# Performance work log

Hardware: AMD Instinct MI355X
Metric: run time of the kernel (lower is better)

The kernel has to match this reference:

```python
import jax, jax.numpy as jnp
import numpy as np

N = 100000          # num_nodes
E = 1250000         # num_edges
H = 64              # node_hidden_size
T = 2               # num_rounds


def setup_inputs() -> dict:
    key = jax.random.key(0)
    ks = jax.random.split(key, 10)
    s = 0.1  # init scale for weights
    return {
        "x": jax.random.normal(ks[0], (N, H), dtype=jnp.float32),
        "edge_index": jax.random.randint(ks[1], (2, E), 0, N, dtype=jnp.int64),
        "edge_attr": jax.random.normal(ks[2], (E, 1), dtype=jnp.float32),
        # message layers: Linear(2H+1 -> H), one per round
        "msg_W": jax.random.normal(ks[3], (T, H, 2 * H + 1), dtype=jnp.float32) * s,
        "msg_b": jax.random.normal(ks[4], (T, H), dtype=jnp.float32) * s,
        # GRUCell params, gate order (r, z, n) as in torch
        "gru_Wih": jax.random.normal(ks[5], (T, 3 * H, H), dtype=jnp.float32) * s,
        "gru_bih": jax.random.normal(ks[6], (T, 3 * H), dtype=jnp.float32) * s,
        "gru_Whh": jax.random.normal(ks[7], (T, 3 * H, H), dtype=jnp.float32) * s,
        "gru_bhh": jax.random.normal(ks[8], (T, 3 * H), dtype=jnp.float32) * s,
    }


def _gru_cell(inp, h, Wih, bih, Whh, bhh):
    # torch.nn.GRUCell math, gate order r, z, n
    gi = inp @ Wih.T + bih   # [N, 3H]
    gh = h @ Whh.T + bhh     # [N, 3H]
    i_r, i_z, i_n = jnp.split(gi, 3, axis=1)
    h_r, h_z, h_n = jnp.split(gh, 3, axis=1)
    r = jax.nn.sigmoid(i_r + h_r)
    z = jax.nn.sigmoid(i_z + h_z)
    n = jnp.tanh(i_n + r * h_n)
    return (1.0 - z) * n + z * h


def reference(x, edge_index, edge_attr, msg_W, msg_b, gru_Wih, gru_bih, gru_Whh, gru_bhh):
    row, col = edge_index[0], edge_index[1]
    num_rounds = msg_W.shape[0]
    for t in range(num_rounds):
        src = x[row]    # [E, H]
        dest = x[col]   # [E, H]
        m_input = jnp.concatenate([dest, src, edge_attr], axis=1)  # [E, 2H+1]
        messages = m_input @ msg_W[t].T + msg_b[t]                 # [E, H]
        agg = jax.ops.segment_sum(messages, row, num_segments=x.shape[0])  # [N, H]
        x = _gru_cell(agg, x, gru_Wih[t], gru_bih[t], gru_Whh[t], gru_bhh[t])
    return x
```

## Files before the change

### kernel.cpp

```cpp
#include <hip/hip_runtime.h>
#include <hip/hip_bf16.h>
#include <hip/hip_fp16.h>

#define H 64
#define CAP 48

typedef __attribute__((ext_vector_type(8))) short short8;
typedef __attribute__((ext_vector_type(4))) float float4v;

__device__ __forceinline__ short f2bf_bits(float f) {
    union { __hip_bfloat16 b; short s; } u;
    u.b = __float2bfloat16(f);
    return u.s;
}
__device__ __forceinline__ float bf2f(unsigned short s) {
    union { unsigned int u; float f; } v;
    v.u = ((unsigned int)s) << 16;
    return v.f;
}
__device__ __forceinline__ void split8(const float* __restrict__ p,
                                       short8& hi, short8& lo) {
    float4v f0 = *(const float4v*)p;
    float4v f1 = *(const float4v*)(p + 4);
#pragma unroll
    for (int j = 0; j < 8; j++) {
        float f = (j < 4) ? f0[j] : f1[j - 4];
        short h = f2bf_bits(f);
        float fh = bf2f((unsigned short)h);
        hi[j] = h;
        lo[j] = f2bf_bits(f - fh);
    }
}
__device__ __forceinline__ void zero8(short8& hi, short8& lo) {
#pragma unroll
    for (int j = 0; j < 8; j++) { hi[j] = 0; lo[j] = 0; }
}

#define MFMA(a, b, c) __builtin_amdgcn_mfma_f32_16x16x32_bf16(a, b, c, 0, 0, 0)

__global__ __launch_bounds__(64) void prep_msg(
    const float* __restrict__ msg_W, short* __restrict__ frag)
{
    const int slot = blockIdx.x & 15, t = blockIdx.x >> 4, lane = threadIdx.x;
    const int tile = slot >> 1, ks = slot & 1;
    const float* W = msg_W + (size_t)t * H * 129;
    const int wrow = (tile & 3) * 16 + (lane & 15);
    const int coff = (tile < 4) ? 0 : 64;
    const int kq = (lane >> 4) * 8;
    short8 hi, lo;
    split8(W + (size_t)wrow * 129 + coff + ks * 32 + kq, hi, lo);
    short8* out = (short8*)(frag + (size_t)t * 16384);
    out[slot * 64 + lane] = hi;
    out[16 * 64 + slot * 64 + lane] = lo;
}

__global__ __launch_bounds__(64) void prep_gru(
    const float* __restrict__ Wih, const float* __restrict__ Whh,
    short* __restrict__ frag)
{
    const int slot = blockIdx.x % 48, t = blockIdx.x / 48, lane = threadIdx.x;
    const int tile = slot >> 1, ks = slot & 1;
    const int kq = (lane >> 4) * 8;
    const float* Wp = (tile < 12)
        ? (Wih + (size_t)t * 192 * H + ((size_t)(tile * 16 + (lane & 15))) * H)
        : (Whh + (size_t)t * 192 * H + ((size_t)((tile - 12) * 16 + (lane & 15))) * H);
    short8 hi, lo;
    split8(Wp + ks * 32 + kq, hi, lo);
    short8* out = (short8*)(frag + (size_t)t * 49152);
    out[slot * 64 + lane] = hi;
    out[48 * 64 + slot * 64 + lane] = lo;
}

__global__ __launch_bounds__(256) void count_cast(
    const int* __restrict__ row, int* __restrict__ deg, int* __restrict__ lpos,
    int E, int EB,
    const float* __restrict__ x_in, __half* __restrict__ xh, int NH8)
{
    if ((int)blockIdx.x < EB) {
        int e = blockIdx.x * 256 + threadIdx.x;
        if (e < E) lpos[e] = atomicAdd(&deg[row[e]], 1);
    } else {
        int i = (blockIdx.x - EB) * 256 + threadIdx.x;
        if (i < NH8) {
            const float* p = x_in + (size_t)i * 8;
            float4v f0 = *(const float4v*)p;
            float4v f1 = *(const float4v*)(p + 4);
            short8 hv;
#pragma unroll
            for (int u = 0; u < 8; u++) {
                float f = (u < 4) ? f0[u] : f1[u - 4];
                hv[u] = __half_as_short(__float2half(f));
            }
            *(short8*)(xh + (size_t)i * 8) = hv;
        }
    }
}

__global__ __launch_bounds__(256) void scatter_bucket(
    const int* __restrict__ row, const int* __restrict__ col,
    const float* __restrict__ attr, const int* __restrict__ lpos,
    int2* __restrict__ edata, int E)
{
    int e = blockIdx.x * 256 + threadIdx.x;
    if (e < E) {
        int p = lpos[e];
        if (p < CAP) {
            int2 v;
            v.x = col[e];
            v.y = __float_as_int(attr[e]);
            edata[(size_t)row[e] * CAP + p] = v;
        }
    }
}

__global__ __launch_bounds__(256) void aggregate(
    const int* __restrict__ deg, const int2* __restrict__ edata,
    const __half* __restrict__ xh,
    short* __restrict__ s_hi, short* __restrict__ s_lo,
    float2* __restrict__ asum2, int N)
{
    const int tid = threadIdx.x, lane = tid & 63, wv = tid >> 6;
    const int n = blockIdx.x * 4 + wv;
    if (n >= N) return;
    int cnt = deg[n];
    if (cnt > CAP) cnt = CAP;
    int2 ed = make_int2(0, 0);
    if (lane < cnt) ed = edata[(size_t)n * CAP + lane];
    const int g = lane >> 3;
    const int cl = lane & 7;
    float acc[8] = {0.f, 0.f, 0.f, 0.f, 0.f, 0.f, 0.f, 0.f};
    float aacc = 0.f;
    for (int j = 0; j < cnt; j += 8) {
        const int idx = j + g;
        int   c = __shfl(ed.x, idx, 64);
        float a = __shfl(__int_as_float(ed.y), idx, 64);
        short8 hv = *(const short8*)(xh + (size_t)c * H + cl * 8);
        if (idx < cnt) {
            aacc += a;
#pragma unroll
            for (int u = 0; u < 8; u++)
                acc[u] += __half2float(__ushort_as_half((unsigned short)hv[u]));
        }
    }
#pragma unroll
    for (int off = 8; off < 64; off <<= 1) {
        aacc += __shfl_xor(aacc, off, 64);
#pragma unroll
        for (int u = 0; u < 8; u++) acc[u] += __shfl_xor(acc[u], off, 64);
    }
    if (lane < 8) {
        short8 hi8, lo8;
#pragma unroll
        for (int u = 0; u < 8; u++) {
            float v = acc[u];
            short h = f2bf_bits(v);
            hi8[u] = h;
            lo8[u] = f2bf_bits(v - bf2f((unsigned short)h));
        }
        *(short8*)(s_hi + (size_t)n * H + lane * 8) = hi8;
        *(short8*)(s_lo + (size_t)n * H + lane * 8) = lo8;
    }
    if (lane == 0) asum2[n] = make_float2(aacc, (float)cnt);
}

#define FSLOT(mt, ks, arr, hl) (((((mt) * 2 + (ks)) * 2 + (arr)) * 2 + (hl)))
__global__ __launch_bounds__(256) void fused_msg_gru(
    const short* __restrict__ s_hi, const short* __restrict__ s_lo,
    const float2* __restrict__ asum2,
    const float* __restrict__ xf,
    float* __restrict__ x, __half* __restrict__ xh,
    const short* __restrict__ mfrag, const short* __restrict__ gfrag,
    const float* __restrict__ Wt, const float* __restrict__ mb,
    const float* __restrict__ bih, const float* __restrict__ bhh,
    int N, int write_xh)
{
    __shared__ short8 afrag[32 * 64];
    const int tid = threadIdx.x, lane = tid & 63, q = tid >> 6;
    const int base = blockIdx.x * 64;
    const int arow = lane & 15;
    const int kq = (lane >> 4) * 8;
    const short8* mhi = (const short8*)mfrag;
    const short8* mlo = mhi + 16 * 64;
    const short8* ghi = (const short8*)gfrag;
    const short8* glo = ghi + 48 * 64;

    {
        const int m = base + q * 16 + arow;
#pragma unroll
        for (int ks = 0; ks < 2; ks++) {
            short8 hi, lo;
            if (m < N) {
                hi = *(const short8*)(s_hi + (size_t)m * H + ks * 32 + kq);
                lo = *(const short8*)(s_lo + (size_t)m * H + ks * 32 + kq);
            } else zero8(hi, lo);
            afrag[FSLOT(q, ks, 0, 0) * 64 + lane] = hi;
            afrag[FSLOT(q, ks, 0, 1) * 64 + lane] = lo;
            if (m < N) split8(xf + (size_t)m * H + ks * 32 + kq, hi, lo);
            else       zero8(hi, lo);
            afrag[FSLOT(q, ks, 1, 0) * 64 + lane] = hi;
            afrag[FSLOT(q, ks, 1, 1) * 64 + lane] = lo;
        }
    }
    __syncthreads();

    float4v accd[4], accs[4];
#pragma unroll
    for (int mt = 0; mt < 4; mt++) {
        accd[mt] = (float4v){0.f, 0.f, 0.f, 0.f};
        accs[mt] = (float4v){0.f, 0.f, 0.f, 0.f};
    }
#pragma unroll
    for (int ks = 0; ks < 2; ks++) {
        short8 ah[4], al[4];
#pragma unroll
        for (int mt = 0; mt < 4; mt++) {
            ah[mt] = afrag[FSLOT(mt, ks, 0, 0) * 64 + lane];
            al[mt] = afrag[FSLOT(mt, ks, 0, 1) * 64 + lane];
        }
        const int sd = q * 2 + ks;
        short8 bh = mhi[sd * 64 + lane];
        short8 bl = mlo[sd * 64 + lane];
#pragma unroll
        for (int mt = 0; mt < 4; mt++) {
            accd[mt] = MFMA(ah[mt], bh, accd[mt]);
            accd[mt] = MFMA(al[mt], bh, accd[mt]);
            accd[mt] = MFMA(ah[mt], bl, accd[mt]);
        }
#pragma unroll
        for (int mt = 0; mt < 4; mt++) {
            ah[mt] = afrag[FSLOT(mt, ks, 1, 0) * 64 + lane];
            al[mt] = afrag[FSLOT(mt, ks, 1, 1) * 64 + lane];
        }
        const int ss = (4 + q) * 2 + ks;
        short8 ch = mhi[ss * 64 + lane];
        short8 cl = mlo[ss * 64 + lane];
#pragma unroll
        for (int mt = 0; mt < 4; mt++) {
            accs[mt] = MFMA(ah[mt], ch, accs[mt]);
            accs[mt] = MFMA(al[mt], ch, accs[mt]);
            accs[mt] = MFMA(ah[mt], cl, accs[mt]);
        }
    }

    const int colb = lane & 15;
    const int rq4 = (lane >> 4) * 4;
    const int j = q * 16 + colb;
    const int ksW  = q >> 1;
    const int quad = (j >> 3) & 3;
    const int elem = j & 7;
    float vv[4][4];
    {
        const float bj = mb[j];
        const float wa = Wt[(size_t)j * 129 + 128];
#pragma unroll
        for (int mt = 0; mt < 4; mt++) {
#pragma unroll
            for (int r = 0; r < 4; r++) {
                const int m = base + mt * 16 + rq4 + r;
                float v = 0.f;
                if (m < N) {
                    float2 da = asum2[m];
                    v = accd[mt][r] + da.y * (accs[mt][r] + bj) + wa * da.x;
                }
                vv[mt][r] = v;
            }
        }
    }
    __syncthreads();

    {
        short* af = (short*)afrag;
#pragma unroll
        for (int mt = 0; mt < 4; mt++) {
#pragma unroll
            for (int r = 0; r < 4; r++) {
                float v = vv[mt][r];
                short hi = f2bf_bits(v);
                float fh = bf2f((unsigned short)hi);
                short lo = f2bf_bits(v - fh);
                const int lane2 = (rq4 + r) | (quad << 4);
                af[(FSLOT(mt, ksW, 0, 0) * 64 + lane2) * 8 + elem] = hi;
                af[(FSLOT(mt, ksW, 0, 1) * 64 + lane2) * 8 + elem] = lo;
            }
        }
    }
    __syncthreads();

    float4v acc[6][4];
#pragma unroll
    for (int g = 0; g < 6; g++)
#pragma unroll
        for (int mt = 0; mt < 4; mt++) acc[g][mt] = (float4v){0.f, 0.f, 0.f, 0.f};

#pragma unroll
    for (int ks = 0; ks < 2; ks++) {
        short8 ah[4], al[4];
#pragma unroll
        for (int mt = 0; mt < 4; mt++) {
            ah[mt] = afrag[FSLOT(mt, ks, 0, 0) * 64 + lane];
            al[mt] = afrag[FSLOT(mt, ks, 0, 1) * 64 + lane];
        }
#pragma unroll
        for (int g = 0; g < 3; g++) {
            const int si = (g * 4 + q) * 2 + ks;
            short8 bh = ghi[si * 64 + lane];
            short8 bl = glo[si * 64 + lane];
#pragma unroll
            for (int mt = 0; mt < 4; mt++) {
                acc[g][mt] = MFMA(ah[mt], bh, acc[g][mt]);
                acc[g][mt] = MFMA(al[mt], bh, acc[g][mt]);
                acc[g][mt] = MFMA(ah[mt], bl, acc[g][mt]);
            }
        }
#pragma unroll
        for (int mt = 0; mt < 4; mt++) {
            ah[mt] = afrag[FSLOT(mt, ks, 1, 0) * 64 + lane];
            al[mt] = afrag[FSLOT(mt, ks, 1, 1) * 64 + lane];
        }
#pragma unroll
        for (int g = 0; g < 3; g++) {
            const int sh = (12 + g * 4 + q) * 2 + ks;
            short8 bh = ghi[sh * 64 + lane];
            short8 bl = glo[sh * 64 + lane];
#pragma unroll
            for (int mt = 0; mt < 4; mt++) {
                acc[3 + g][mt] = MFMA(ah[mt], bh, acc[3 + g][mt]);
                acc[3 + g][mt] = MFMA(al[mt], bh, acc[3 + g][mt]);
                acc[3 + g][mt] = MFMA(ah[mt], bl, acc[3 + g][mt]);
            }
        }
    }

    const float b_ir = bih[j], b_iz = bih[64 + j], b_in = bih[128 + j];
    const float b_hr = bhh[j], b_hz = bhh[64 + j], b_hn = bhh[128 + j];
    const short* af = (const short*)afrag;
#pragma unroll
    for (int mt = 0; mt < 4; mt++) {
#pragma unroll
        for (int r = 0; r < 4; r++) {
            const int m = base + mt * 16 + rq4 + r;
            if (m >= N) continue;
            float ir = acc[0][mt][r] + b_ir;
            float iz = acc[1][mt][r] + b_iz;
            float in_ = acc[2][mt][r] + b_in;
            float hr = acc[3][mt][r] + b_hr;
            float hz = acc[4][mt][r] + b_hz;
            float hn = acc[5][mt][r] + b_hn;
            float rr = 1.f / (1.f + __expf(-(ir + hr)));
            float zz = 1.f / (1.f + __expf(-(iz + hz)));
            float e2 = __expf(2.f * (in_ + rr * hn));
            float nn = 1.f - 2.f / (e2 + 1.f);
            const int lane2 = (rq4 + r) | (quad << 4);
            float hold = bf2f((unsigned short)af[(FSLOT(mt, ksW, 1, 0) * 64 + lane2) * 8 + elem])
                       + bf2f((unsigned short)af[(FSLOT(mt, ksW, 1, 1) * 64 + lane2) * 8 + elem]);
            float out = (1.f - zz) * nn + zz * hold;
            x[(size_t)m * H + j] = out;
            if (write_xh) xh[(size_t)m * H + j] = __float2half(out);
        }
    }
}

extern "C" void kernel_launch(void* const* d_in, const int* in_sizes, int n_in,
                              void* d_out, int out_size, void* d_ws, size_t ws_size,
                              hipStream_t stream) {
    const float* x_in  = (const float*)d_in[0];
    const int*   ei    = (const int*)d_in[1];
    const float* attr  = (const float*)d_in[2];
    const float* msg_W = (const float*)d_in[3];
    const float* msg_b = (const float*)d_in[4];
    const float* Wih   = (const float*)d_in[5];
    const float* bih   = (const float*)d_in[6];
    const float* Whh   = (const float*)d_in[7];
    const float* bhh   = (const float*)d_in[8];

    const int N = in_sizes[0] / H;
    const int E = in_sizes[2];
    const int T = in_sizes[4] / H;
    const int* row = ei;
    const int* col = ei + E;

    float*  x       = (float*)d_out;
    short*  s_hi    = (short*)d_ws;
    short*  s_lo    = s_hi + (size_t)N * H;
    int*    lpos    = (int*)s_lo;
    __half* xh      = (__half*)(s_lo + (size_t)N * H);
    float2* asum2   = (float2*)(xh + (size_t)N * H);
    int*    deg     = (int*)(asum2 + N);
    int2*   edata   = (int2*)(deg + N);
    short*  msgfrag = (short*)(edata + (size_t)N * CAP);
    short*  grufrag = msgfrag + (size_t)T * 16384;

    const int eb  = (E + 255) / 256;
    const int nh8 = (N * H) / 8;
    const int cb  = (nh8 + 255) / 256;

    hipMemsetAsync(deg, 0, (size_t)N * sizeof(int), stream);

    prep_msg<<<T * 16, 64, 0, stream>>>(msg_W, msgfrag);
    prep_gru<<<T * 48, 64, 0, stream>>>(Wih, Whh, grufrag);

    count_cast<<<eb + cb, 256, 0, stream>>>(row, deg, lpos, E, eb, x_in, xh, nh8);
    scatter_bucket<<<eb, 256, 0, stream>>>(row, col, attr, lpos, edata, E);

    const int nbq        = (N + 63) / 64;
    const int agg_blocks = (N + 3) / 4;

    for (int t = 0; t < T; t++) {
        aggregate<<<agg_blocks, 256, 0, stream>>>(
            deg, edata, xh, s_hi, s_lo, asum2, N);
        fused_msg_gru<<<nbq, 256, 0, stream>>>(
            s_hi, s_lo, asum2,
            (t == 0) ? x_in : x, x, xh,
            msgfrag + (size_t)t * 16384, grufrag + (size_t)t * 49152,
            msg_W + (size_t)t * H * (2 * H + 1), msg_b + (size_t)t * H,
            bih + (size_t)t * 3 * H, bhh + (size_t)t * 3 * H,
            N, (t + 1 < T) ? 1 : 0);
    }
}
```

Before: 361.5 us.

## Merge prep kernels, use 8-lane-per-node aggregation, make msg-GRU kernel per-wave

The weight-fragment prep kernels are folded into the degree-count launch, and the fp16 cast of x moves into the scatter launch, cutting the launch count. Aggregation now gives each node 8 lanes that loop over its edges sequentially, replacing a 64-lane wave per node with shuffles and a cross-lane reduction. The fused message+GRU kernel is restructured so each wave owns 16 rows and all output columns, keeping A fragments in registers, using per-wave LDS scratch instead of block-wide shared fragments and __syncthreads, and reading the old hidden state directly from fp32 x. The trade-offs are more weight-fragment global loads per wave, longer serial per-lane loops for high-degree nodes, and dropped __restrict__ on the x pointers.

```diff
diff --git a/kernel.cpp b/kernel.cpp
--- a/kernel.cpp
+++ b/kernel.cpp
@@ -18,8 +18,7 @@
     v.u = ((unsigned int)s) << 16;
     return v.f;
 }
-__device__ __forceinline__ void split8(const float* __restrict__ p,
-                                       short8& hi, short8& lo) {
+__device__ __forceinline__ void split8(const float* p, short8& hi, short8& lo) {
     float4v f0 = *(const float4v*)p;
     float4v f1 = *(const float4v*)(p + 4);
 #pragma unroll
@@ -38,47 +37,65 @@
 
 #define MFMA(a, b, c) __builtin_amdgcn_mfma_f32_16x16x32_bf16(a, b, c, 0, 0, 0)
 
-__global__ __launch_bounds__(64) void prep_msg(
-    const float* __restrict__ msg_W, short* __restrict__ frag)
-{
-    const int slot = blockIdx.x & 15, t = blockIdx.x >> 4, lane = threadIdx.x;
-    const int tile = slot >> 1, ks = slot & 1;
-    const float* W = msg_W + (size_t)t * H * 129;
-    const int wrow = (tile & 3) * 16 + (lane & 15);
-    const int coff = (tile < 4) ? 0 : 64;
-    const int kq = (lane >> 4) * 8;
-    short8 hi, lo;
-    split8(W + (size_t)wrow * 129 + coff + ks * 32 + kq, hi, lo);
-    short8* out = (short8*)(frag + (size_t)t * 16384);
-    out[slot * 64 + lane] = hi;
-    out[16 * 64 + slot * 64 + lane] = lo;
-}
-
-__global__ __launch_bounds__(64) void prep_gru(
-    const float* __restrict__ Wih, const float* __restrict__ Whh,
-    short* __restrict__ frag)
-{
-    const int slot = blockIdx.x % 48, t = blockIdx.x / 48, lane = threadIdx.x;
-    const int tile = slot >> 1, ks = slot & 1;
-    const int kq = (lane >> 4) * 8;
-    const float* Wp = (tile < 12)
-        ? (Wih + (size_t)t * 192 * H + ((size_t)(tile * 16 + (lane & 15))) * H)
-        : (Whh + (size_t)t * 192 * H + ((size_t)((tile - 12) * 16 + (lane & 15))) * H);
-    short8 hi, lo;
-    split8(Wp + ks * 32 + kq, hi, lo);
-    short8* out = (short8*)(frag + (size_t)t * 49152);
-    out[slot * 64 + lane] = hi;
-    out[48 * 64 + slot * 64 + lane] = lo;
-}
-
-__global__ __launch_bounds__(256) void count_cast(
+__global__ __launch_bounds__(256) void count_prep(
     const int* __restrict__ row, int* __restrict__ deg, int* __restrict__ lpos,
     int E, int EB,
+    const float* __restrict__ msg_W,
+    const float* __restrict__ Wih, const float* __restrict__ Whh,
+    short* __restrict__ msgfrag, short* __restrict__ grufrag, int T)
+{
+    if ((int)blockIdx.x < EB) {
+        int e = blockIdx.x * 256 + threadIdx.x;
+        if (e < E) lpos[e] = atomicAdd(&deg[row[e]], 1);
+        return;
+    }
+    const int lane = threadIdx.x & 63;
+    int unit = (blockIdx.x - EB) * 4 + (threadIdx.x >> 6);
+    const int kq = (lane >> 4) * 8;
+    if (unit < T * 16) {
+        const int slot = unit & 15, t = unit >> 4;
+        const int tile = slot >> 1, ks = slot & 1;
+        const float* W = msg_W + (size_t)t * H * 129;
+        const int wrow = (tile & 3) * 16 + (lane & 15);
+        const int coff = (tile < 4) ? 0 : 64;
+        short8 hi, lo;
+        split8(W + (size_t)wrow * 129 + coff + ks * 32 + kq, hi, lo);
+        short8* out = (short8*)(msgfrag + (size_t)t * 16384);
+        out[slot * 64 + lane] = hi;
+        out[16 * 64 + slot * 64 + lane] = lo;
+    } else {
+        unit -= T * 16;
+        if (unit >= T * 48) return;
+        const int slot = unit % 48, t = unit / 48;
+        const int tile = slot >> 1, ks = slot & 1;
+        const float* Wp = (tile < 12)
+            ? (Wih + (size_t)t * 192 * H + ((size_t)(tile * 16 + (lane & 15))) * H)
+            : (Whh + (size_t)t * 192 * H + ((size_t)((tile - 12) * 16 + (lane & 15))) * H);
+        short8 hi, lo;
+        split8(Wp + ks * 32 + kq, hi, lo);
+        short8* out = (short8*)(grufrag + (size_t)t * 49152);
+        out[slot * 64 + lane] = hi;
+        out[48 * 64 + slot * 64 + lane] = lo;
+    }
+}
+
+__global__ __launch_bounds__(256) void scatter_cast(
+    const int* __restrict__ row, const int* __restrict__ col,
+    const float* __restrict__ attr, const int* __restrict__ lpos,
+    int2* __restrict__ edata, int E, int EB,
     const float* __restrict__ x_in, __half* __restrict__ xh, int NH8)
 {
     if ((int)blockIdx.x < EB) {
         int e = blockIdx.x * 256 + threadIdx.x;
-        if (e < E) lpos[e] = atomicAdd(&deg[row[e]], 1);
+        if (e < E) {
+            int p = lpos[e];
+            if (p < CAP) {
+                int2 v;
+                v.x = col[e];
+                v.y = __float_as_int(attr[e]);
+                edata[(size_t)row[e] * CAP + p] = v;
+            }
+        }
     } else {
         int i = (blockIdx.x - EB) * 256 + threadIdx.x;
         if (i < NH8) {
@@ -96,23 +113,6 @@
     }
 }
 
-__global__ __launch_bounds__(256) void scatter_bucket(
-    const int* __restrict__ row, const int* __restrict__ col,
-    const float* __restrict__ attr, const int* __restrict__ lpos,
-    int2* __restrict__ edata, int E)
-{
-    int e = blockIdx.x * 256 + threadIdx.x;
-    if (e < E) {
-        int p = lpos[e];
-        if (p < CAP) {
-            int2 v;
-            v.x = col[e];
-            v.y = __float_as_int(attr[e]);
-            edata[(size_t)row[e] * CAP + p] = v;
-        }
-    }
-}
-
 __global__ __launch_bounds__(256) void aggregate(
     const int* __restrict__ deg, const int2* __restrict__ edata,
     const __half* __restrict__ xh,
@@ -120,35 +120,22 @@
     float2* __restrict__ asum2, int N)
 {
     const int tid = threadIdx.x, lane = tid & 63, wv = tid >> 6;
-    const int n = blockIdx.x * 4 + wv;
-    if (n >= N) return;
-    int cnt = deg[n];
-    if (cnt > CAP) cnt = CAP;
-    int2 ed = make_int2(0, 0);
-    if (lane < cnt) ed = edata[(size_t)n * CAP + lane];
-    const int g = lane >> 3;
-    const int cl = lane & 7;
+    const int g = lane >> 3, cl = lane & 7;
+    const int n = (blockIdx.x * 4 + wv) * 8 + g;
+    int cnt = 0;
+    if (n < N) { cnt = deg[n]; if (cnt > CAP) cnt = CAP; }
+    const int2* ebase = edata + (size_t)n * CAP;
     float acc[8] = {0.f, 0.f, 0.f, 0.f, 0.f, 0.f, 0.f, 0.f};
     float aacc = 0.f;
-    for (int j = 0; j < cnt; j += 8) {
-        const int idx = j + g;
-        int   c = __shfl(ed.x, idx, 64);
-        float a = __shfl(__int_as_float(ed.y), idx, 64);
-        short8 hv = *(const short8*)(xh + (size_t)c * H + cl * 8);
-        if (idx < cnt) {
-            aacc += a;
-#pragma unroll
-            for (int u = 0; u < 8; u++)
-                acc[u] += __half2float(__ushort_as_half((unsigned short)hv[u]));
-        }
-    }
-#pragma unroll
-    for (int off = 8; off < 64; off <<= 1) {
-        aacc += __shfl_xor(aacc, off, 64);
-#pragma unroll
-        for (int u = 0; u < 8; u++) acc[u] += __shfl_xor(acc[u], off, 64);
-    }
-    if (lane < 8) {
+    for (int j = 0; j < cnt; j++) {
+        int2 ed = ebase[j];
+        aacc += __int_as_float(ed.y);
+        short8 hv = *(const short8*)(xh + (size_t)ed.x * H + cl * 8);
+#pragma unroll
+        for (int u = 0; u < 8; u++)
+            acc[u] += __half2float(__ushort_as_half((unsigned short)hv[u]));
+    }
+    if (n < N) {
         short8 hi8, lo8;
 #pragma unroll
         for (int u = 0; u < 8; u++) {
@@ -157,202 +144,136 @@
             hi8[u] = h;
             lo8[u] = f2bf_bits(v - bf2f((unsigned short)h));
         }
-        *(short8*)(s_hi + (size_t)n * H + lane * 8) = hi8;
-        *(short8*)(s_lo + (size_t)n * H + lane * 8) = lo8;
-    }
-    if (lane == 0) asum2[n] = make_float2(aacc, (float)cnt);
-}
-
-#define FSLOT(mt, ks, arr, hl) (((((mt) * 2 + (ks)) * 2 + (arr)) * 2 + (hl)))
+        *(short8*)(s_hi + (size_t)n * H + cl * 8) = hi8;
+        *(short8*)(s_lo + (size_t)n * H + cl * 8) = lo8;
+        if (cl == 0) asum2[n] = make_float2(aacc, (float)cnt);
+    }
+}
+
 __global__ __launch_bounds__(256) void fused_msg_gru(
     const short* __restrict__ s_hi, const short* __restrict__ s_lo,
     const float2* __restrict__ asum2,
-    const float* __restrict__ xf,
-    float* __restrict__ x, __half* __restrict__ xh,
+    const float* xf,
+    float* x, __half* __restrict__ xh,
     const short* __restrict__ mfrag, const short* __restrict__ gfrag,
     const float* __restrict__ Wt, const float* __restrict__ mb,
     const float* __restrict__ bih, const float* __restrict__ bhh,
     int N, int write_xh)
 {
-    __shared__ short8 afrag[32 * 64];
-    const int tid = threadIdx.x, lane = tid & 63, q = tid >> 6;
-    const int base = blockIdx.x * 64;
+    __shared__ float scratch[4][16 * 68];
+    const int tid = threadIdx.x, lane = tid & 63, wv = tid >> 6;
+    const int base = blockIdx.x * 64 + wv * 16;
+    if (base >= N) return;
     const int arow = lane & 15;
     const int kq = (lane >> 4) * 8;
+    const int colb = lane & 15;
+    const int rq4 = (lane >> 4) * 4;
+    const int m_a = base + arow;
+    const bool mv = (m_a < N);
     const short8* mhi = (const short8*)mfrag;
     const short8* mlo = mhi + 16 * 64;
     const short8* ghi = (const short8*)gfrag;
     const short8* glo = ghi + 48 * 64;
 
-    {
-        const int m = base + q * 16 + arow;
-#pragma unroll
-        for (int ks = 0; ks < 2; ks++) {
-            short8 hi, lo;
-            if (m < N) {
-                hi = *(const short8*)(s_hi + (size_t)m * H + ks * 32 + kq);
-                lo = *(const short8*)(s_lo + (size_t)m * H + ks * 32 + kq);
-            } else zero8(hi, lo);
-            afrag[FSLOT(q, ks, 0, 0) * 64 + lane] = hi;
-            afrag[FSLOT(q, ks, 0, 1) * 64 + lane] = lo;
-            if (m < N) split8(xf + (size_t)m * H + ks * 32 + kq, hi, lo);
-            else       zero8(hi, lo);
-            afrag[FSLOT(q, ks, 1, 0) * 64 + lane] = hi;
-            afrag[FSLOT(q, ks, 1, 1) * 64 + lane] = lo;
-        }
-    }
-    __syncthreads();
+    short8 sfh[2], sfl[2], xfh[2], xfl[2];
+#pragma unroll
+    for (int ks = 0; ks < 2; ks++) {
+        if (mv) {
+            sfh[ks] = *(const short8*)(s_hi + (size_t)m_a * H + ks * 32 + kq);
+            sfl[ks] = *(const short8*)(s_lo + (size_t)m_a * H + ks * 32 + kq);
+            split8(xf + (size_t)m_a * H + ks * 32 + kq, xfh[ks], xfl[ks]);
+        } else { zero8(sfh[ks], sfl[ks]); zero8(xfh[ks], xfl[ks]); }
+    }
+    float2 da[4];
+#pragma unroll
+    for (int r = 0; r < 4; r++) {
+        const int m = base + rq4 + r;
+        da[r] = (m < N) ? asum2[m] : make_float2(0.f, 0.f);
+    }
 
     float4v accd[4], accs[4];
 #pragma unroll
-    for (int mt = 0; mt < 4; mt++) {
-        accd[mt] = (float4v){0.f, 0.f, 0.f, 0.f};
-        accs[mt] = (float4v){0.f, 0.f, 0.f, 0.f};
+    for (int ct = 0; ct < 4; ct++) {
+        accd[ct] = (float4v){0.f, 0.f, 0.f, 0.f};
+        accs[ct] = (float4v){0.f, 0.f, 0.f, 0.f};
     }
 #pragma unroll
     for (int ks = 0; ks < 2; ks++) {
-        short8 ah[4], al[4];
-#pragma unroll
-        for (int mt = 0; mt < 4; mt++) {
-            ah[mt] = afrag[FSLOT(mt, ks, 0, 0) * 64 + lane];
-            al[mt] = afrag[FSLOT(mt, ks, 0, 1) * 64 + lane];
-        }
-        const int sd = q * 2 + ks;
-        short8 bh = mhi[sd * 64 + lane];
-        short8 bl = mlo[sd * 64 + lane];
-#pragma unroll
-        for (int mt = 0; mt < 4; mt++) {
-            accd[mt] = MFMA(ah[mt], bh, accd[mt]);
-            accd[mt] = MFMA(al[mt], bh, accd[mt]);
-            accd[mt] = MFMA(ah[mt], bl, accd[mt]);
-        }
-#pragma unroll
-        for (int mt = 0; mt < 4; mt++) {
-            ah[mt] = afrag[FSLOT(mt, ks, 1, 0) * 64 + lane];
-            al[mt] = afrag[FSLOT(mt, ks, 1, 1) * 64 + lane];
-        }
-        const int ss = (4 + q) * 2 + ks;
-        short8 ch = mhi[ss * 64 + lane];
-        short8 cl = mlo[ss * 64 + lane];
-#pragma unroll
-        for (int mt = 0; mt < 4; mt++) {
-            accs[mt] = MFMA(ah[mt], ch, accs[mt]);
-            accs[mt] = MFMA(al[mt], ch, accs[mt]);
-            accs[mt] = MFMA(ah[mt], cl, accs[mt]);
-        }
-    }
-
-    const int colb = lane & 15;
-    const int rq4 = (lane >> 4) * 4;
-    const int j = q * 16 + colb;
-    const int ksW  = q >> 1;
-    const int quad = (j >> 3) & 3;
-    const int elem = j & 7;
-    float vv[4][4];
-    {
+#pragma unroll
+        for (int ct = 0; ct < 4; ct++) {
+            short8 bh = mhi[(ct * 2 + ks) * 64 + lane];
+            short8 bl = mlo[(ct * 2 + ks) * 64 + lane];
+            accd[ct] = MFMA(sfh[ks], bh, accd[ct]);
+            accd[ct] = MFMA(sfl[ks], bh, accd[ct]);
+            accd[ct] = MFMA(sfh[ks], bl, accd[ct]);
+            short8 ch = mhi[((4 + ct) * 2 + ks) * 64 + lane];
+            short8 cl8 = mlo[((4 + ct) * 2 + ks) * 64 + lane];
+            accs[ct] = MFMA(xfh[ks], ch, accs[ct]);
+            accs[ct] = MFMA(xfl[ks], ch, accs[ct]);
+            accs[ct] = MFMA(xfh[ks], cl8, accs[ct]);
+        }
+    }
+
+    float* scr = scratch[wv];
+#pragma unroll
+    for (int ct = 0; ct < 4; ct++) {
+        const int j = ct * 16 + colb;
         const float bj = mb[j];
         const float wa = Wt[(size_t)j * 129 + 128];
 #pragma unroll
-        for (int mt = 0; mt < 4; mt++) {
-#pragma unroll
-            for (int r = 0; r < 4; r++) {
-                const int m = base + mt * 16 + rq4 + r;
-                float v = 0.f;
-                if (m < N) {
-                    float2 da = asum2[m];
-                    v = accd[mt][r] + da.y * (accs[mt][r] + bj) + wa * da.x;
-                }
-                vv[mt][r] = v;
+        for (int r = 0; r < 4; r++) {
+            float v = accd[ct][r] + da[r].y * (accs[ct][r] + bj) + da[r].x * wa;
+            scr[(rq4 + r) * 68 + j] = v;
+        }
+    }
+    asm volatile("s_waitcnt lgkmcnt(0)" ::: "memory");
+    short8 agh[2], agl[2];
+#pragma unroll
+    for (int ks = 0; ks < 2; ks++)
+        split8(scr + arow * 68 + ks * 32 + kq, agh[ks], agl[ks]);
+
+#pragma unroll
+    for (int ct = 0; ct < 4; ct++) {
+        float4v ai[3], ao[3];
+#pragma unroll
+        for (int g2 = 0; g2 < 3; g2++) {
+            ai[g2] = (float4v){0.f, 0.f, 0.f, 0.f};
+            ao[g2] = (float4v){0.f, 0.f, 0.f, 0.f};
+        }
+#pragma unroll
+        for (int ks = 0; ks < 2; ks++) {
+#pragma unroll
+            for (int g2 = 0; g2 < 3; g2++) {
+                short8 bh = ghi[((g2 * 4 + ct) * 2 + ks) * 64 + lane];
+                short8 bl = glo[((g2 * 4 + ct) * 2 + ks) * 64 + lane];
+                ai[g2] = MFMA(agh[ks], bh, ai[g2]);
+                ai[g2] = MFMA(agl[ks], bh, ai[g2]);
+                ai[g2] = MFMA(agh[ks], bl, ai[g2]);
+                short8 hh = ghi[((12 + g2 * 4 + ct) * 2 + ks) * 64 + lane];
+                short8 hl = glo[((12 + g2 * 4 + ct) * 2 + ks) * 64 + lane];
+                ao[g2] = MFMA(xfh[ks], hh, ao[g2]);
+                ao[g2] = MFMA(xfl[ks], hh, ao[g2]);
+                ao[g2] = MFMA(xfh[ks], hl, ao[g2]);
             }
         }
-    }
-    __syncthreads();
-
-    {
-        short* af = (short*)afrag;
-#pragma unroll
-        for (int mt = 0; mt < 4; mt++) {
-#pragma unroll
-            for (int r = 0; r < 4; r++) {
-                float v = vv[mt][r];
-                short hi = f2bf_bits(v);
-                float fh = bf2f((unsigned short)hi);
-                short lo = f2bf_bits(v - fh);
-                const int lane2 = (rq4 + r) | (quad << 4);
-                af[(FSLOT(mt, ksW, 0, 0) * 64 + lane2) * 8 + elem] = hi;
-                af[(FSLOT(mt, ksW, 0, 1) * 64 + lane2) * 8 + elem] = lo;
-            }
-        }
-    }
-    __syncthreads();
-
-    float4v acc[6][4];
-#pragma unroll
-    for (int g = 0; g < 6; g++)
-#pragma unroll
-        for (int mt = 0; mt < 4; mt++) acc[g][mt] = (float4v){0.f, 0.f, 0.f, 0.f};
-
-#pragma unroll
-    for (int ks = 0; ks < 2; ks++) {
-        short8 ah[4], al[4];
-#pragma unroll
-        for (int mt = 0; mt < 4; mt++) {
-            ah[mt] = afrag[FSLOT(mt, ks, 0, 0) * 64 + lane];
-            al[mt] = afrag[FSLOT(mt, ks, 0, 1) * 64 + lane];
-        }
-#pragma unroll
-        for (int g = 0; g < 3; g++) {
-            const int si = (g * 4 + q) * 2 + ks;
-            short8 bh = ghi[si * 64 + lane];
-            short8 bl = glo[si * 64 + lane];
-#pragma unroll
-            for (int mt = 0; mt < 4; mt++) {
-                acc[g][mt] = MFMA(ah[mt], bh, acc[g][mt]);
-                acc[g][mt] = MFMA(al[mt], bh, acc[g][mt]);
-                acc[g][mt] = MFMA(ah[mt], bl, acc[g][mt]);
-            }
-        }
-#pragma unroll
-        for (int mt = 0; mt < 4; mt++) {
-            ah[mt] = afrag[FSLOT(mt, ks, 1, 0) * 64 + lane];
-            al[mt] = afrag[FSLOT(mt, ks, 1, 1) * 64 + lane];
-        }
-#pragma unroll
-        for (int g = 0; g < 3; g++) {
-            const int sh = (12 + g * 4 + q) * 2 + ks;
-            short8 bh = ghi[sh * 64 + lane];
-            short8 bl = glo[sh * 64 + lane];
-#pragma unroll
-            for (int mt = 0; mt < 4; mt++) {
-                acc[3 + g][mt] = MFMA(ah[mt], bh, acc[3 + g][mt]);
-                acc[3 + g][mt] = MFMA(al[mt], bh, acc[3 + g][mt]);
-                acc[3 + g][mt] = MFMA(ah[mt], bl, acc[3 + g][mt]);
-            }
-        }
-    }
-
-    const float b_ir = bih[j], b_iz = bih[64 + j], b_in = bih[128 + j];
-    const float b_hr = bhh[j], b_hz = bhh[64 + j], b_hn = bhh[128 + j];
-    const short* af = (const short*)afrag;
-#pragma unroll
-    for (int mt = 0; mt < 4; mt++) {
+        const int j = ct * 16 + colb;
+        const float b_ir = bih[j], b_iz = bih[64 + j], b_in = bih[128 + j];
+        const float b_hr = bhh[j], b_hz = bhh[64 + j], b_hn = bhh[128 + j];
 #pragma unroll
         for (int r = 0; r < 4; r++) {
-            const int m = base + mt * 16 + rq4 + r;
+            const int m = base + rq4 + r;
             if (m >= N) continue;
-            float ir = acc[0][mt][r] + b_ir;
-            float iz = acc[1][mt][r] + b_iz;
-            float in_ = acc[2][mt][r] + b_in;
-            float hr = acc[3][mt][r] + b_hr;
-            float hz = acc[4][mt][r] + b_hz;
-            float hn = acc[5][mt][r] + b_hn;
+            float ir = ai[0][r] + b_ir;
+            float iz = ai[1][r] + b_iz;
+            float in_ = ai[2][r] + b_in;
+            float hr = ao[0][r] + b_hr;
+            float hz = ao[1][r] + b_hz;
+            float hn = ao[2][r] + b_hn;
             float rr = 1.f / (1.f + __expf(-(ir + hr)));
             float zz = 1.f / (1.f + __expf(-(iz + hz)));
             float e2 = __expf(2.f * (in_ + rr * hn));
             float nn = 1.f - 2.f / (e2 + 1.f);
-            const int lane2 = (rq4 + r) | (quad << 4);
-            float hold = bf2f((unsigned short)af[(FSLOT(mt, ksW, 1, 0) * 64 + lane2) * 8 + elem])
-                       + bf2f((unsigned short)af[(FSLOT(mt, ksW, 1, 1) * 64 + lane2) * 8 + elem]);
+            float hold = xf[(size_t)m * H + j];
             float out = (1.f - zz) * nn + zz * hold;
             x[(size_t)m * H + j] = out;
             if (write_xh) xh[(size_t)m * H + j] = __float2half(out);
@@ -393,17 +314,17 @@
     const int eb  = (E + 255) / 256;
     const int nh8 = (N * H) / 8;
     const int cb  = (nh8 + 255) / 256;
+    const int pb  = (T * 16 + T * 48 + 3) / 4;
 
     hipMemsetAsync(deg, 0, (size_t)N * sizeof(int), stream);
 
-    prep_msg<<<T * 16, 64, 0, stream>>>(msg_W, msgfrag);
-    prep_gru<<<T * 48, 64, 0, stream>>>(Wih, Whh, grufrag);
-
-    count_cast<<<eb + cb, 256, 0, stream>>>(row, deg, lpos, E, eb, x_in, xh, nh8);
-    scatter_bucket<<<eb, 256, 0, stream>>>(row, col, attr, lpos, edata, E);
+    count_prep<<<eb + pb, 256, 0, stream>>>(
+        row, deg, lpos, E, eb, msg_W, Wih, Whh, msgfrag, grufrag, T);
+    scatter_cast<<<eb + cb, 256, 0, stream>>>(
+        row, col, attr, lpos, edata, E, eb, x_in, xh, nh8);
 
     const int nbq        = (N + 63) / 64;
-    const int agg_blocks = (N + 3) / 4;
+    const int agg_blocks = (N + 31) / 32;
 
     for (int t = 0; t < T; t++) {
         aggregate<<<agg_blocks, 256, 0, stream>>>(
```

After: 352.9 us. 1.02x faster.
